# Kernel tuning notes

Measured on AMD Instinct MI355X. Metric: run time of the kernel, lower is better.

Reference implementation:

```python
import jax, jax.numpy as jnp
import numpy as np

SCORE_THRESH = 0.5
NMS_THRESH = 0.4
TOP_K = 1000  # fixed pre-NMS candidate budget (jit-safe replacement for boolean masking)
STRIDES = (8, 16, 32)
H, W = 2176, 3840


def _anchor_centers(fh, fw, stride):
    yv, xv = jnp.meshgrid(jnp.arange(fh), jnp.arange(fw), indexing='ij')
    return (jnp.stack([xv, yv], -1).reshape(-1, 2).astype(jnp.float32)) * stride  # [N,2]


def _decode_level(scores, bbox, kps, stride):
    fh, fw = H // stride, W // stride
    c = _anchor_centers(fh, fw, stride)                 # [N,2]
    s = jax.nn.sigmoid(scores.reshape(-1))              # [N]
    d = bbox.reshape(-1, 4) * stride                    # [N,4]
    boxes = jnp.concatenate([c - d[:, :2], c + d[:, 2:4]], axis=1)  # x1y1x2y2
    k = kps.reshape(-1, 5, 2) * stride + c[:, None, :]  # (x,y) pairs
    return s, boxes, k.reshape(-1, 10)


def _iou_matrix(b):
    area = (b[:, 2] - b[:, 0]) * (b[:, 3] - b[:, 1])
    lt = jnp.maximum(b[:, None, :2], b[None, :, :2])
    rb = jnp.minimum(b[:, None, 2:], b[None, :, 2:])
    wh = jnp.clip(rb - lt, 0.0)
    inter = wh[..., 0] * wh[..., 1]
    return inter / jnp.clip(area[:, None] + area[None, :] - inter, 1e-9)


def _nms_keep(iou, valid):
    n = iou.shape[0]
    ar = jnp.arange(n)

    def body(i, keep):
        sup = (iou[i] > NMS_THRESH) & (ar > i) & keep[i]
        return keep & ~sup

    return jax.lax.fori_loop(0, n, body, valid)


def reference(x, scores8, bbox8, kps8, scores16, bbox16, kps16, scores32, bbox32, kps32):
    levels = ((scores8, bbox8, kps8), (scores16, bbox16, kps16), (scores32, bbox32, kps32))
    ss, bs, ks = [], [], []
    for (s, b, k), stride in zip(levels, STRIDES):
        si, bi, ki = _decode_level(s, b, k, stride)
        ss.append(si); bs.append(bi); ks.append(ki)
    scores = jnp.concatenate(ss)   # [N_total]
    boxes = jnp.concatenate(bs)    # [N_total,4]
    kpss = jnp.concatenate(ks)     # [N_total,10]

    masked = jnp.where(scores > SCORE_THRESH, scores, -1.0)
    top_s, idx = jax.lax.top_k(masked, TOP_K)
    valid = top_s > SCORE_THRESH
    b = boxes[idx]
    k = kpss[idx]

    keep = jax.lax.stop_gradient(_nms_keep(_iou_matrix(b), valid))
    final_boxes = jnp.where(keep[:, None], b, 0.0)
    final_scores = jnp.where(keep, top_s, 0.0)
    final_kpss = jnp.where(keep[:, None], k, 0.0)
    return final_boxes, final_scores, final_kpss


def setup_inputs() -> dict:
    key = jax.random.key(0)
    ks = jax.random.split(key, 10)
    n8 = (H // 8) * (W // 8)
    n16 = (H // 16) * (W // 16)
    n32 = (H // 32) * (W // 32)
    return {
        'x': jax.random.normal(ks[0], (1, 3, H, W), jnp.float32),
        'scores8': jax.random.normal(ks[1], (1, n8, 1), jnp.float32),
        'bbox8': jax.random.uniform(ks[2], (1, n8, 4), jnp.float32),
        'kps8': jax.random.normal(ks[3], (1, n8, 10), jnp.float32),
        'scores16': jax.random.normal(ks[4], (1, n16, 1), jnp.float32),
        'bbox16': jax.random.uniform(ks[5], (1, n16, 4), jnp.float32),
        'kps16': jax.random.normal(ks[6], (1, n16, 10), jnp.float32),
        'scores32': jax.random.normal(ks[7], (1, n32, 1), jnp.float32),
        'bbox32': jax.random.uniform(ks[8], (1, n32, 4), jnp.float32),
        'kps32': jax.random.normal(ks[9], (1, n32, 10), jnp.float32),
    }
```

## Files before the change

### kernel.cpp

```cpp
#include <hip/hip_runtime.h>
#include <stdint.h>

typedef unsigned int u32;
typedef unsigned long long u64;

#define N8   130560
#define N16  32640
#define N32  8160
#define NTOT 171360
#define NTOT4 42840
#define TOPK 1000
#define NWORDS 16
#define NBINS 4096
#define BUCKET_SCALE 682.0f
#define LIST_CAP 2016
#define CPB 32
#define HIST_BLKS 84
#define HIST_THR 512
#define RED_BLKS 32
#define CMP_BLKS 168
#define RANK_BLKS 63
#define IOU_BLKS 63
#define IOU_TASKS (TOPK * NWORDS)
#define NMS_CACHE 256
#define POISON 0xAAAAAAAAu


#define MI_CNT 0
#define MI_IOU 128
#define META_U32 256

#define OFF_PART 0
#define OFF_RED  688128
#define OFF_META 704512
#define OFF_NZ   705536
#define OFF_LIST 705664
#define OFF_MASK 721792

__device__ __forceinline__ u32 ald32(const u32* p) {
  return __hip_atomic_load(p, __ATOMIC_RELAXED, __HIP_MEMORY_SCOPE_AGENT);
}
__device__ __forceinline__ u64 ald64(const u64* p) {
  return __hip_atomic_load(p, __ATOMIC_RELAXED, __HIP_MEMORY_SCOPE_AGENT);
}
__device__ __forceinline__ void ast64(u64* p, u64 v) {
  __hip_atomic_store(p, v, __ATOMIC_RELAXED, __HIP_MEMORY_SCOPE_AGENT);
}

__device__ __forceinline__ u32 bucket_of(float x) {
  u32 b = (u32)(x * BUCKET_SCALE);
  return b > (NBINS - 1) ? (NBINS - 1) : b;
}

__device__ __forceinline__ float4 load_logit4(int v, const float* s8, const float* s16,
                                              const float* s32) {
  int e = v * 4;
  if (e < N8) return ((const float4*)s8)[v];
  if (e < N8 + N16) return ((const float4*)s16)[v - N8 / 4];
  return ((const float4*)s32)[v - (N8 + N16) / 4];
}

__device__ __forceinline__ bool iou_gt04(float4 a, float4 b) {
#pragma clang fp contract(off)
  float areaA = (a.z - a.x) * (a.w - a.y);
  float areaB = (b.z - b.x) * (b.w - b.y);
  float ltx = fmaxf(a.x, b.x);
  float lty = fmaxf(a.y, b.y);
  float rbx = fminf(a.z, b.z);
  float rby = fminf(a.w, b.w);
  float wx = rbx - ltx; wx = wx > 0.0f ? wx : 0.0f;
  float wy = rby - lty; wy = wy > 0.0f ? wy : 0.0f;
  float inter = wx * wy;
  float un = areaA + areaB - inter;
  un = un > 1e-9f ? un : 1e-9f;
  return (inter / un) > 0.4f;
}

__device__ __forceinline__ u64 valid_word(int w, u32 vcnt) {
  int lo = w * 64;
  if ((int)vcnt >= lo + 64) return ~0ull;
  if ((int)vcnt <= lo) return 0ull;
  return (1ull << (vcnt - (u32)lo)) - 1ull;
}

__global__ void __launch_bounds__(HIST_THR) k1_hist(
    const float* __restrict__ s8, const float* __restrict__ s16, const float* __restrict__ s32,
    u32* __restrict__ part, u32* __restrict__ meta, u64* __restrict__ nz) {
  __shared__ u32 lh[NBINS];
  const int t = threadIdx.x, blk = blockIdx.x;
#pragma unroll
  for (int k = 0; k < 8; ++k) lh[k * HIST_THR + t] = 0;
  __syncthreads();
  int v = blk * HIST_THR + t;
  if (v < NTOT4) {
    float4 x = load_logit4(v, s8, s16, s32);
    if (x.x > 0.0f) atomicAdd(&lh[bucket_of(x.x)], 1u);
    if (x.y > 0.0f) atomicAdd(&lh[bucket_of(x.y)], 1u);
    if (x.z > 0.0f) atomicAdd(&lh[bucket_of(x.z)], 1u);
    if (x.w > 0.0f) atomicAdd(&lh[bucket_of(x.w)], 1u);
  }
  __syncthreads();
#pragma unroll
  for (int k = 0; k < 4; ++k) {
    int w = k * HIST_THR + t;
    part[blk * 2048 + w] = lh[2 * w] | (lh[2 * w + 1] << 16);
  }
  if (blk == 0) {
    if (t < META_U32) meta[t] = 0;
    if (t < NWORDS) nz[t] = 0ull;
  }
}

__global__ void __launch_bounds__(256) k2_reduce(
    const u32* __restrict__ part, u32* __restrict__ red) {
  __shared__ u32 llo[256], lhi[256];
  const int t = threadIdx.x, blk = blockIdx.x;
  const int w = t & 63, pp = t >> 6;
  u32 lo = 0, hi = 0;
  for (int p = pp; p < HIST_BLKS; p += 4) {
    u32 pv = part[p * 2048 + blk * 64 + w];
    lo += pv & 0xFFFFu; hi += pv >> 16;
  }
  llo[t] = lo; lhi[t] = hi;
  __syncthreads();
  if (t < 64) {
    u32 l = llo[t] + llo[64 + t] + llo[128 + t] + llo[192 + t];
    u32 h = lhi[t] + lhi[64 + t] + lhi[128 + t] + lhi[192 + t];
    red[blk * 128 + 2 * t] = l;
    red[blk * 128 + 2 * t + 1] = h;
  }
}

__global__ void __launch_bounds__(256) k4_compact(
    const float* __restrict__ s8, const float* __restrict__ s16, const float* __restrict__ s32,
    const u32* __restrict__ red, u32* __restrict__ meta, u64* __restrict__ list) {
  __shared__ u32 hloc[NBINS];
  __shared__ u32 csum[256];
  __shared__ u32 sB, sBase;
  __shared__ u32 cnt16[16];
  const int t = threadIdx.x, blk = blockIdx.x;
  const int wave = t >> 6, lane = t & 63;
  const int v = blk * 256 + t;
  float4 x = make_float4(-1.f, -1.f, -1.f, -1.f);
  if (v < NTOT4) x = load_logit4(v, s8, s16, s32);
#pragma unroll
  for (int k = 0; k < 16; ++k) hloc[k * 256 + t] = red[k * 256 + t];
  __syncthreads();
  u32 sum = 0;
  int base = t * 16;
#pragma unroll
  for (int k = 0; k < 16; ++k) sum += hloc[base + k];
  csum[t] = sum;
  __syncthreads();
  for (int off = 1; off < 256; off <<= 1) {
    u32 add = (t + off < 256) ? csum[t + off] : 0u;
    __syncthreads();
    csum[t] += add;
    __syncthreads();
  }
  u32 above = (t < 255) ? csum[t + 1] : 0u;
  if (t == 0 && csum[0] < TOPK) sB = 0u;
  if (csum[t] >= TOPK && above < TOPK) {
    u32 cum = above, Bv = (u32)(t * 16);
    for (int b = t * 16 + 15; b >= t * 16; --b) {
      cum += hloc[b];
      if (cum >= TOPK) { Bv = (u32)b; break; }
    }
    sB = Bv;
  }
  __syncthreads();
  const u32 B = sB;
  float c[4] = {x.x, x.y, x.z, x.w};
  u32 win = 0;
#pragma unroll
  for (int j = 0; j < 4; ++j)
    if (c[j] > 0.0f && bucket_of(c[j]) >= B) win |= 1u << j;
  u32 wpos[4], wcnt[4];
#pragma unroll
  for (int j = 0; j < 4; ++j) {
    u64 bal = __ballot((win >> j) & 1u);
    wcnt[j] = (u32)__popcll(bal);
    wpos[j] = (u32)__popcll(bal & ((1ull << lane) - 1ull));
  }
  if (lane == 0) {
#pragma unroll
    for (int j = 0; j < 4; ++j) cnt16[wave * 4 + j] = wcnt[j];
  }
  __syncthreads();
  if (t == 0) {
    u32 tot = 0, pre[16];
#pragma unroll
    for (int k = 0; k < 16; ++k) { pre[k] = tot; tot += cnt16[k]; }
#pragma unroll
    for (int k = 0; k < 16; ++k) cnt16[k] = pre[k];
    sBase = tot ? atomicAdd(&meta[MI_CNT], tot) : 0u;
  }
  __syncthreads();
#pragma unroll
  for (int j = 0; j < 4; ++j) {
    if ((win >> j) & 1u) {
      u32 dst = sBase + cnt16[wave * 4 + j] + wpos[j];
      if (dst < LIST_CAP) {
        u32 idx = (u32)(v * 4 + j);
        list[dst] = ((u64)__float_as_uint(c[j]) << 32) | (u64)(~idx);
      }
    }
  }
}

__global__ void __launch_bounds__(256) k5_rank(
    const u32* __restrict__ meta, const u64* __restrict__ list,
    const float* __restrict__ bb8,  const float* __restrict__ kp8,
    const float* __restrict__ bb16, const float* __restrict__ kp16,
    const float* __restrict__ bb32, const float* __restrict__ kp32,
    float* __restrict__ out) {
  __shared__ __align__(16) u64 keys[LIST_CAP];
  __shared__ u32 rpart[256];
  __shared__ u32 sCnt;
  const int t = threadIdx.x, blk = blockIdx.x;
  if (t == 0) { u32 cc = meta[MI_CNT]; sCnt = cc > LIST_CAP ? LIST_CAP : cc; }
  __syncthreads();
  const u32 cnt = sCnt;
  for (int j = t; j < LIST_CAP; j += 256) keys[j] = (j < (int)cnt) ? list[j] : 0ull;
  __syncthreads();
  {
    const int ci = t & 31, sl = t >> 5;
    const int c = blk * CPB + ci;
    const int chunk = ((int)cnt + 7) >> 3;
    int lo = sl * chunk; if (lo > (int)cnt) lo = (int)cnt;
    int hi = lo + chunk; if (hi > (int)cnt) hi = (int)cnt;
    u64 my = keys[c];
    int r = 0, j = lo;
    for (; j + 4 <= hi; j += 4)
      r += (keys[j] > my) + (keys[j + 1] > my) + (keys[j + 2] > my) + (keys[j + 3] > my);
    for (; j < hi; ++j) r += (keys[j] > my);
    rpart[t] = (u32)r;
  }
  __syncthreads();
  if (t < CPB) {
    const int c = blk * CPB + t;
    if (c < (int)cnt) {
      int rank = 0;
#pragma unroll
      for (int q = 0; q < 8; ++q) rank += (int)rpart[t + 32 * q];
      if (rank < TOPK) {
        u64 my = keys[c];
        float lx = __uint_as_float((u32)(my >> 32));
        float sc = (float)(1.0 / (1.0 + exp(-(double)lx)));
        u32 idx = ~((u32)my);
        float4 box;
        float kv[10];
        int p, xq, yq;
        float st;
        const float *bb, *kp;
        if (idx < N8) {
          st = 8.f;  p = (int)idx;              xq = p % 480; yq = p / 480; bb = bb8;  kp = kp8;
        } else if (idx < N8 + N16) {
          st = 16.f; p = (int)idx - N8;         xq = p % 240; yq = p / 240; bb = bb16; kp = kp16;
        } else {
          st = 32.f; p = (int)idx - (N8 + N16); xq = p % 120; yq = p / 120; bb = bb32; kp = kp32;
        }
        float cx = (float)xq * st, cy = (float)yq * st;
        {
#pragma clang fp contract(off)
          float d0 = bb[4 * p + 0] * st;
          float d1 = bb[4 * p + 1] * st;
          float d2 = bb[4 * p + 2] * st;
          float d3 = bb[4 * p + 3] * st;
          box.x = cx - d0; box.y = cy - d1; box.z = cx + d2; box.w = cy + d3;
          for (int q = 0; q < 10; ++q)
            kv[q] = kp[10 * p + q] * st + ((q & 1) ? cy : cx);
        }
        ((float4*)out)[rank] = box;
        out[4000 + rank] = sc;
#pragma unroll
        for (int q = 0; q < 10; ++q) out[5000 + 10 * rank + q] = kv[q];
      }
    } else if (c < TOPK) {
      ((float4*)out)[c] = make_float4(0.f, 0.f, 0.f, 0.f);
      out[4000 + c] = 0.f;
#pragma unroll
      for (int q = 0; q < 10; ++q) out[5000 + 10 * c + q] = 0.f;
    }
  }
}

__global__ void __launch_bounds__(256) k67_iou_nms(
    u32* meta, u64* nzWords, u64* mask, float* out) {
  __shared__ __align__(16) char smem[36864];
  __shared__ int isLast;
  __shared__ u32 sPc[16], sOff17[17];
  __shared__ u64 sRem[NWORDS];
  const int t = threadIdx.x, blk = blockIdx.x;

  float4* boxes = (float4*)smem;
  for (int r = t; r < TOPK; r += 256) boxes[r] = ((const float4*)out)[r];
  __syncthreads();
  int task = blk * 256 + t;
  if (task < IOU_TASKS) {
    int w = task / 1000;
    int i = task - w * 1000;
    float4 a = boxes[i];
    int bse = w * 64;
    int jend = (bse + 64) < TOPK ? (bse + 64) : TOPK;
    u64 bits = 0;
    for (int j = bse; j < jend; ++j)
      if (j > i && iou_gt04(a, boxes[j])) bits |= 1ull << (j - bse);
    ast64(&mask[(u64)w * 1000 + i], bits);
    if (bits) atomicOr(&nzWords[i >> 6], 1ull << (i & 63));
  }
  __syncthreads();
  if (t == 0)
    isLast = (__hip_atomic_fetch_add(&meta[MI_IOU], 1u, __ATOMIC_RELAXED,
                                     __HIP_MEMORY_SCOPE_AGENT) == (u32)(IOU_BLKS - 1));
  __syncthreads();
  if (!isLast) return;

  u32 cc = meta[MI_CNT];
  if (cc > LIST_CAP) cc = LIST_CAP;
  const u32 vcnt = cc < TOPK ? cc : TOPK;
  u32* rows = (u32*)smem;
  u64* cache = (u64*)(smem + 4096);
  u64 nzv = 0;
  if (t < NWORDS) {
    nzv = ald64(&nzWords[t]) & valid_word(t, vcnt);
    sPc[t] = (u32)__popcll(nzv);
  }
  __syncthreads();
  if (t == 0) {
    u32 o = 0;
    for (int w = 0; w < NWORDS; ++w) { sOff17[w] = o; o += sPc[w]; }
    sOff17[16] = o;
  }
  __syncthreads();
  if (t < NWORDS) {
    u64 m = nzv;
    u32 o = sOff17[t];
    while (m) { int b = __builtin_ctzll(m); m &= m - 1; rows[o++] = (u32)(t * 64 + b); }
  }
  __syncthreads();
  const int S = (int)sOff17[16];
  const int Sc = S < NMS_CACHE ? S : NMS_CACHE;
  for (int idx = t; idx < Sc * NWORDS; idx += 256) {
    int s = idx >> 4, w = idx & 15;
    cache[s * NWORDS + w] = ald64(&mask[(u64)w * 1000 + rows[s]]);
  }
  __syncthreads();
  if (t < 64) {
    u64 remv = 0;
    for (int s = 0; s < S; ++s) {
      u32 row = rows[s];
      int c = (int)(row >> 6), b = (int)(row & 63);
      u64 remc = __shfl(remv, c);
      if (!((remc >> b) & 1ull)) {
        u64 m = 0;
        if (t < NWORDS)
          m = (s < NMS_CACHE) ? cache[s * NWORDS + t] : ald64(&mask[(u64)t * 1000 + row]);
        remv |= m;
      }
    }
    if (t < NWORDS) sRem[t] = valid_word(t, vcnt) & remv;
  }
  __syncthreads();
  for (int r = t; r < TOPK; r += 256) {
    if ((sRem[r >> 6] >> (r & 63)) & 1ull) {
      ((float4*)out)[r] = make_float4(0.f, 0.f, 0.f, 0.f);
      out[4000 + r] = 0.f;
#pragma unroll
      for (int q = 0; q < 10; ++q) out[5000 + 10 * r + q] = 0.f;
    }
  }
}

extern "C" void kernel_launch(void* const* d_in, const int* in_sizes, int n_in,
                              void* d_out, int out_size, void* d_ws, size_t ws_size,
                              hipStream_t stream) {
  const float* s8   = (const float*)d_in[1];
  const float* bb8  = (const float*)d_in[2];
  const float* kp8  = (const float*)d_in[3];
  const float* s16  = (const float*)d_in[4];
  const float* bb16 = (const float*)d_in[5];
  const float* kp16 = (const float*)d_in[6];
  const float* s32  = (const float*)d_in[7];
  const float* bb32 = (const float*)d_in[8];
  const float* kp32 = (const float*)d_in[9];

  char* ws = (char*)d_ws;
  u32* part    = (u32*)(ws + OFF_PART);
  u32* red     = (u32*)(ws + OFF_RED);
  u32* meta    = (u32*)(ws + OFF_META);
  u64* nzWords = (u64*)(ws + OFF_NZ);
  u64* list    = (u64*)(ws + OFF_LIST);
  u64* mask    = (u64*)(ws + OFF_MASK);
  float* out   = (float*)d_out;

  k1_hist<<<HIST_BLKS, HIST_THR, 0, stream>>>(s8, s16, s32, part, meta, nzWords);
  k2_reduce<<<RED_BLKS, 256, 0, stream>>>(part, red);
  k4_compact<<<CMP_BLKS, 256, 0, stream>>>(s8, s16, s32, red, meta, list);
  k5_rank<<<RANK_BLKS, 256, 0, stream>>>(meta, list, bb8, kp8, bb16, kp16, bb32, kp32, out);
  k67_iou_nms<<<IOU_BLKS, 256, 0, stream>>>(meta, nzWords, mask, out);
}
```

Measured before the change: 170.6 us.

## Fold histogram reduction and threshold search into histogram kernel via last-block arrival

Removes the separate reduce kernel. The last histogram block to arrive, detected with an atomic counter, now sums the per-block partial histograms, runs the prefix scan and writes the bucket threshold to meta. The histogram shrinks from 4096 to 512 bins, and the compact kernel reads one threshold value instead of having all 168 blocks reload and scan the full histogram. This saves a kernel launch, redundant scans and workspace traffic. In exchange, coarser bins admit more candidates above the threshold, and cross-block visibility depends on relaxed atomics with no explicit fences.

```diff
diff --git a/kernel.cpp b/kernel.cpp
--- a/kernel.cpp
+++ b/kernel.cpp
@@ -11,13 +11,12 @@
 #define NTOT4 42840
 #define TOPK 1000
 #define NWORDS 16
-#define NBINS 4096
-#define BUCKET_SCALE 682.0f
+#define NBINS 512
+#define BUCKET_SCALE 85.25f
 #define LIST_CAP 2016
 #define CPB 32
 #define HIST_BLKS 84
 #define HIST_THR 512
-#define RED_BLKS 32
 #define CMP_BLKS 168
 #define RANK_BLKS 63
 #define IOU_BLKS 63
@@ -28,14 +27,16 @@
 
 #define MI_CNT 0
 #define MI_IOU 128
-#define META_U32 256
+#define MI_ARR 256
+#define MI_B   384
+#define META_U32 512
+#define META_ZERO 256
 
 #define OFF_PART 0
-#define OFF_RED  688128
-#define OFF_META 704512
-#define OFF_NZ   705536
-#define OFF_LIST 705664
-#define OFF_MASK 721792
+#define OFF_META 86016
+#define OFF_NZ   88064
+#define OFF_LIST 88192
+#define OFF_MASK 104320
 
 __device__ __forceinline__ u32 ald32(const u32* p) {
   return __hip_atomic_load(p, __ATOMIC_RELAXED, __HIP_MEMORY_SCOPE_AGENT);
@@ -43,8 +44,19 @@
 __device__ __forceinline__ u64 ald64(const u64* p) {
   return __hip_atomic_load(p, __ATOMIC_RELAXED, __HIP_MEMORY_SCOPE_AGENT);
 }
+__device__ __forceinline__ void ast32(u32* p, u32 v) {
+  __hip_atomic_store(p, v, __ATOMIC_RELAXED, __HIP_MEMORY_SCOPE_AGENT);
+}
 __device__ __forceinline__ void ast64(u64* p, u64 v) {
   __hip_atomic_store(p, v, __ATOMIC_RELAXED, __HIP_MEMORY_SCOPE_AGENT);
+}
+__device__ __forceinline__ u32 normc(u32 v) {
+  return v >= 0x80000000u ? v - POISON : v;
+}
+__device__ __forceinline__ bool arrive_last(u32* p, u32 total) {
+  u32 old = __hip_atomic_fetch_add(p, 1u, __ATOMIC_RELAXED, __HIP_MEMORY_SCOPE_AGENT);
+  if (normc(old) == total - 1u) { ast32(p, 0u); return true; }
+  return false;
 }
 
 __device__ __forceinline__ u32 bucket_of(float x) {
@@ -85,11 +97,12 @@
 
 __global__ void __launch_bounds__(HIST_THR) k1_hist(
     const float* __restrict__ s8, const float* __restrict__ s16, const float* __restrict__ s32,
-    u32* __restrict__ part, u32* __restrict__ meta, u64* __restrict__ nz) {
+    u32* __restrict__ part, u32* meta, u64* __restrict__ nz) {
   __shared__ u32 lh[NBINS];
+  __shared__ u32 csum[256];
+  __shared__ int sLast;
   const int t = threadIdx.x, blk = blockIdx.x;
-#pragma unroll
-  for (int k = 0; k < 8; ++k) lh[k * HIST_THR + t] = 0;
+  lh[t < NBINS ? t : 0] = 0;
   __syncthreads();
   int v = blk * HIST_THR + t;
   if (v < NTOT4) {
@@ -100,74 +113,63 @@
     if (x.w > 0.0f) atomicAdd(&lh[bucket_of(x.w)], 1u);
   }
   __syncthreads();
-#pragma unroll
-  for (int k = 0; k < 4; ++k) {
-    int w = k * HIST_THR + t;
-    part[blk * 2048 + w] = lh[2 * w] | (lh[2 * w + 1] << 16);
-  }
+  if (t < 256)
+    ast32(&part[blk * 256 + t], lh[2 * t] | (lh[2 * t + 1] << 16));
   if (blk == 0) {
-    if (t < META_U32) meta[t] = 0;
+    if (t < META_ZERO) meta[t] = 0;
     if (t < NWORDS) nz[t] = 0ull;
   }
-}
-
-__global__ void __launch_bounds__(256) k2_reduce(
-    const u32* __restrict__ part, u32* __restrict__ red) {
-  __shared__ u32 llo[256], lhi[256];
-  const int t = threadIdx.x, blk = blockIdx.x;
-  const int w = t & 63, pp = t >> 6;
+  __syncthreads();
+  if (t == 0) sLast = arrive_last(&meta[MI_ARR], HIST_BLKS) ? 1 : 0;
+  __syncthreads();
+  if (!sLast) return;
+
   u32 lo = 0, hi = 0;
-  for (int p = pp; p < HIST_BLKS; p += 4) {
-    u32 pv = part[p * 2048 + blk * 64 + w];
-    lo += pv & 0xFFFFu; hi += pv >> 16;
-  }
-  llo[t] = lo; lhi[t] = hi;
-  __syncthreads();
-  if (t < 64) {
-    u32 l = llo[t] + llo[64 + t] + llo[128 + t] + llo[192 + t];
-    u32 h = lhi[t] + lhi[64 + t] + lhi[128 + t] + lhi[192 + t];
-    red[blk * 128 + 2 * t] = l;
-    red[blk * 128 + 2 * t + 1] = h;
+  if (t < 256) {
+    int p = 0;
+    for (; p + 4 <= HIST_BLKS; p += 4) {
+      u32 a0 = ald32(&part[(p + 0) * 256 + t]);
+      u32 a1 = ald32(&part[(p + 1) * 256 + t]);
+      u32 a2 = ald32(&part[(p + 2) * 256 + t]);
+      u32 a3 = ald32(&part[(p + 3) * 256 + t]);
+      lo += (a0 & 0xFFFFu) + (a1 & 0xFFFFu) + (a2 & 0xFFFFu) + (a3 & 0xFFFFu);
+      hi += (a0 >> 16) + (a1 >> 16) + (a2 >> 16) + (a3 >> 16);
+    }
+    for (; p < HIST_BLKS; ++p) {
+      u32 a = ald32(&part[p * 256 + t]);
+      lo += a & 0xFFFFu; hi += a >> 16;
+    }
+  }
+  __syncthreads();
+  if (t < 256) { lh[2 * t] = lo; lh[2 * t + 1] = hi; csum[t] = lo + hi; }
+  __syncthreads();
+  for (int off = 1; off < 256; off <<= 1) {
+    u32 add = (t < 256 && t + off < 256) ? csum[t + off] : 0u;
+    __syncthreads();
+    if (t < 256) csum[t] += add;
+    __syncthreads();
+  }
+  if (t == 0 && csum[0] < TOPK) meta[MI_B] = 0u;
+  if (t < 256) {
+    u32 above = (t < 255) ? csum[t + 1] : 0u;
+    if (csum[t] >= TOPK && above < TOPK) {
+      u32 cum = above + lh[2 * t + 1];
+      meta[MI_B] = (cum >= TOPK) ? (u32)(2 * t + 1) : (u32)(2 * t);
+    }
   }
 }
 
 __global__ void __launch_bounds__(256) k4_compact(
     const float* __restrict__ s8, const float* __restrict__ s16, const float* __restrict__ s32,
-    const u32* __restrict__ red, u32* __restrict__ meta, u64* __restrict__ list) {
-  __shared__ u32 hloc[NBINS];
-  __shared__ u32 csum[256];
+    u32* __restrict__ meta, u64* __restrict__ list) {
   __shared__ u32 sB, sBase;
   __shared__ u32 cnt16[16];
   const int t = threadIdx.x, blk = blockIdx.x;
   const int wave = t >> 6, lane = t & 63;
   const int v = blk * 256 + t;
+  if (t == 0) sB = meta[MI_B];
   float4 x = make_float4(-1.f, -1.f, -1.f, -1.f);
   if (v < NTOT4) x = load_logit4(v, s8, s16, s32);
-#pragma unroll
-  for (int k = 0; k < 16; ++k) hloc[k * 256 + t] = red[k * 256 + t];
-  __syncthreads();
-  u32 sum = 0;
-  int base = t * 16;
-#pragma unroll
-  for (int k = 0; k < 16; ++k) sum += hloc[base + k];
-  csum[t] = sum;
-  __syncthreads();
-  for (int off = 1; off < 256; off <<= 1) {
-    u32 add = (t + off < 256) ? csum[t + off] : 0u;
-    __syncthreads();
-    csum[t] += add;
-    __syncthreads();
-  }
-  u32 above = (t < 255) ? csum[t + 1] : 0u;
-  if (t == 0 && csum[0] < TOPK) sB = 0u;
-  if (csum[t] >= TOPK && above < TOPK) {
-    u32 cum = above, Bv = (u32)(t * 16);
-    for (int b = t * 16 + 15; b >= t * 16; --b) {
-      cum += hloc[b];
-      if (cum >= TOPK) { Bv = (u32)b; break; }
-    }
-    sB = Bv;
-  }
   __syncthreads();
   const u32 B = sB;
   float c[4] = {x.x, x.y, x.z, x.w};
@@ -387,7 +389,6 @@
 
   char* ws = (char*)d_ws;
   u32* part    = (u32*)(ws + OFF_PART);
-  u32* red     = (u32*)(ws + OFF_RED);
   u32* meta    = (u32*)(ws + OFF_META);
   u64* nzWords = (u64*)(ws + OFF_NZ);
   u64* list    = (u64*)(ws + OFF_LIST);
@@ -395,8 +396,7 @@
   float* out   = (float*)d_out;
 
   k1_hist<<<HIST_BLKS, HIST_THR, 0, stream>>>(s8, s16, s32, part, meta, nzWords);
-  k2_reduce<<<RED_BLKS, 256, 0, stream>>>(part, red);
-  k4_compact<<<CMP_BLKS, 256, 0, stream>>>(s8, s16, s32, red, meta, list);
+  k4_compact<<<CMP_BLKS, 256, 0, stream>>>(s8, s16, s32, meta, list);
   k5_rank<<<RANK_BLKS, 256, 0, stream>>>(meta, list, bb8, kp8, bb16, kp16, bb32, kp32, out);
   k67_iou_nms<<<IOU_BLKS, 256, 0, stream>>>(meta, nzWords, mask, out);
 }
```

Result: no change. 169.7 us (-0.5%).
